# Performance work log

Measured on AMD Instinct MI355X. Metric: run time of the kernel, lower is better.

## Reference

```python
import jax, jax.numpy as jnp
import numpy as np

VOL_SHAPE = (256, 256, 256)
DELTA = 1
EPS = 1e-8


def _radius_bins(shape, delta):
    # Frequency-index radius map (equivalent to distance from DC with fft wraparound),
    # binned into shells of width `delta`. Computed once with numpy (constant).
    axes = [np.fft.fftfreq(n) * n for n in shape]
    grids = np.meshgrid(*axes, indexing='ij')
    r = np.sqrt(sum(g.astype(np.float64) ** 2 for g in grids))
    bins = np.floor(r / delta).astype(np.int32)
    return bins.ravel(), int(bins.max()) + 1

_BINS, _NUM_SHELLS = _radius_bins(VOL_SHAPE, DELTA)
_BINS_J = jnp.asarray(_BINS)


def setup_inputs() -> dict:
    key = jax.random.key(0)
    kx, ky = jax.random.split(key)
    shp = (2, 1) + VOL_SHAPE
    X = jax.random.normal(kx, shp, dtype=jnp.float32)
    Y = jax.random.normal(ky, shp, dtype=jnp.float32)
    return {"X": X, "Y": Y}


def _fsc(X, Y):
    B, C = X.shape[0], X.shape[1]
    Fx = jnp.fft.fftn(X, axes=(-3, -2, -1))  # complex64 [B,C,D,H,W]
    Fy = jnp.fft.fftn(Y, axes=(-3, -2, -1))
    N = VOL_SHAPE[0] * VOL_SHAPE[1] * VOL_SHAPE[2]
    # Per-voxel quantities, flattened over the volume: [B*C, N]
    num = (Fx.real * Fy.real + Fx.imag * Fy.imag).reshape(B * C, N)  # Re(Fx * conj(Fy))
    px = (Fx.real ** 2 + Fx.imag ** 2).reshape(B * C, N)
    py = (Fy.real ** 2 + Fy.imag ** 2).reshape(B * C, N)
    seg = lambda v: jax.ops.segment_sum(v, _BINS_J, num_segments=_NUM_SHELLS)
    num_s = jax.vmap(seg)(num)  # [B*C, S]
    px_s = jax.vmap(seg)(px)
    py_s = jax.vmap(seg)(py)
    fsc = num_s / jnp.sqrt(px_s * py_s + EPS)  # [B*C, S]
    return fsc.reshape(B, C, _NUM_SHELLS)


def reference(X, Y):
    fsc = _fsc(X, Y)
    # size_average=True: average over radii, channel and batch -> scalar
    return jnp.mean(fsc)
```

## Files before the change

### kernel.cpp

```cpp
#include <hip/hip_runtime.h>
#include <math.h>

#define VOL (256 * 256 * 256)
#define NSHELL 222
#define SBINS 224
#define NSPLIT 16
#define PI_D 3.14159265358979323846
#define VSTRIDE ((size_t)129 << 16)

__global__ void tw_init(float2* __restrict__ gtw) {
  int t = threadIdx.x;
  double a = -2.0 * PI_D * (double)t / 256.0;
  gtw[t] = make_float2((float)cos(a), (float)sin(a));
}

__device__ __forceinline__ void seg_flush(float* sh, int sb, float nv, float pv,
                                          float qv, int l) {
#pragma unroll
  for (int d = 1; d < 64; d <<= 1) {
    int sbo = __shfl_down(sb, d);
    float no = __shfl_down(nv, d);
    float po = __shfl_down(pv, d);
    float qo = __shfl_down(qv, d);
    if (l + d < 64 && sbo == sb) { nv += no; pv += po; qv += qo; }
  }
  int sbp = __shfl_up(sb, 1);
  if (l == 0 || sbp != sb) {
    atomicAdd(&sh[3 * sb + 0], nv);
    atomicAdd(&sh[3 * sb + 1], pv);
    atomicAdd(&sh[3 * sb + 2], qv);
  }
}

__device__ __forceinline__ float2 cmul(float2 a, float2 b) {
  return make_float2(a.x * b.x - a.y * b.y, a.x * b.y + a.y * b.x);
}

__device__ __forceinline__ void fft16(float2* v) {
  const float C1 = 0.92387953251128674f;
  const float S1 = 0.38268343236508978f;
  const float R2 = 0.70710678118654752f;
  float2 s[16];
#pragma unroll
  for (int p = 0; p < 4; ++p) {
    float2 a = v[p], b = v[p + 4], cc = v[p + 8], d = v[p + 12];
    float2 t0 = make_float2(a.x + cc.x, a.y + cc.y);
    float2 t2 = make_float2(a.x - cc.x, a.y - cc.y);
    float2 t1 = make_float2(b.x + d.x, b.y + d.y);
    float2 t3 = make_float2(b.x - d.x, b.y - d.y);
    s[p]      = make_float2(t0.x + t1.x, t0.y + t1.y);
    s[p + 4]  = make_float2(t2.x + t3.y, t2.y - t3.x);
    s[p + 8]  = make_float2(t0.x - t1.x, t0.y - t1.y);
    s[p + 12] = make_float2(t2.x - t3.y, t2.y + t3.x);
  }
  s[5]  = cmul(s[5],  make_float2(C1, -S1));
  s[6]  = cmul(s[6],  make_float2(R2, -R2));
  s[7]  = cmul(s[7],  make_float2(S1, -C1));
  s[9]  = cmul(s[9],  make_float2(R2, -R2));
  s[10] = cmul(s[10], make_float2(0.f, -1.f));
  s[11] = cmul(s[11], make_float2(-R2, -R2));
  s[13] = cmul(s[13], make_float2(S1, -C1));
  s[14] = cmul(s[14], make_float2(-R2, -R2));
  s[15] = cmul(s[15], make_float2(-C1, S1));
#pragma unroll
  for (int r = 0; r < 4; ++r) {
    float2 u0 = s[4 * r], u1 = s[4 * r + 1], u2 = s[4 * r + 2], u3 = s[4 * r + 3];
    float2 e0 = make_float2(u0.x + u2.x, u0.y + u2.y);
    float2 e1 = make_float2(u0.x - u2.x, u0.y - u2.y);
    float2 o0 = make_float2(u1.x + u3.x, u1.y + u3.y);
    float2 o1 = make_float2(u1.x - u3.x, u1.y - u3.y);
    v[r]      = make_float2(e0.x + o0.x, e0.y + o0.y);
    v[4 + r]  = make_float2(e1.x + o1.y, e1.y - o1.x);
    v[8 + r]  = make_float2(e0.x - o0.x, e0.y - o0.y);
    v[12 + r] = make_float2(e1.x - o1.y, e1.y + o1.x);
  }
}

__global__ __launch_bounds__(256, 4) void fft_z_pack(const float* __restrict__ X,
                                                     const float* __restrict__ Y,
                                                     float2* __restrict__ Gx,
                                                     float2* __restrict__ Gy,
                                                     const float2* __restrict__ gtw) {
  __shared__ float2 zs[256 * 17];
  int t = threadIdx.x;
  int li = t >> 4, c = t & 15;
  int y = blockIdx.x >> 4;
  int x0 = (blockIdx.x & 15) << 4;
  const float4* xp = (const float4*)(X + (((size_t)(x0 + li)) << 16) + ((size_t)y << 8));
  const float4* yp = (const float4*)(Y + (((size_t)(x0 + li)) << 16) + ((size_t)y << 8));
#pragma unroll
  for (int it = 0; it < 4; ++it) {
    float4 a = xp[c + 16 * it];
    float4 b = yp[c + 16 * it];
    int z0 = 4 * c + 64 * it;
    zs[(z0 + 0) * 17 + li] = make_float2(a.x, b.x);
    zs[(z0 + 1) * 17 + li] = make_float2(a.y, b.y);
    zs[(z0 + 2) * 17 + li] = make_float2(a.z, b.z);
    zs[(z0 + 3) * 17 + li] = make_float2(a.w, b.w);
  }
  float2 v[16];
#pragma unroll
  for (int m = 0; m < 16; ++m) v[m] = zs[(16 * m + c) * 17 + li];
  fft16(v);
#pragma unroll
  for (int k1 = 1; k1 < 16; ++k1) v[k1] = cmul(v[k1], gtw[c * k1]);
#pragma unroll
  for (int k1 = 0; k1 < 16; ++k1) zs[(16 * c + ((k1 + c) & 15)) * 17 + li] = v[k1];
  float2 u[16];
#pragma unroll
  for (int j2 = 0; j2 < 16; ++j2) u[j2] = zs[(16 * j2 + ((c + j2) & 15)) * 17 + li];
  fft16(u);
#pragma unroll
  for (int k2 = 0; k2 < 16; ++k2) zs[(16 * k2 + c) * 17 + li] = u[k2];
  __syncthreads();
  int xo = t & 15, ko = t >> 4;
  float2* gx = Gx + ((size_t)y << 8) + (size_t)(x0 + xo);
  float2* gy = Gy + ((size_t)y << 8) + (size_t)(x0 + xo);
#pragma unroll
  for (int g = 0; g < 9; ++g) {
    int kz = 16 * g + ko;
    if (kz <= 128) {
      float2 a = zs[kz * 17 + xo];
      float2 b = zs[((256 - kz) & 255) * 17 + xo];
      size_t off = (size_t)kz << 16;
      gx[off] = make_float2(0.5f * (a.x + b.x), 0.5f * (a.y - b.y));
      gy[off] = make_float2(0.5f * (a.y + b.y), 0.5f * (b.x - a.x));
    }
  }
}

__global__ __launch_bounds__(256, 4) void fft_y(float2* __restrict__ G,
                                                const float2* __restrict__ gtw) {
  __shared__ float2 scr[16 * 273];
  int t = threadIdx.x;
  int xi = t & 15, h = t >> 4;
  int x0 = blockIdx.x << 4;
  int kz = blockIdx.y;
  float2* Gp = G + (size_t)blockIdx.z * VSTRIDE + ((size_t)kz << 16) + (size_t)(x0 + xi);
  float2 v[16];
#pragma unroll
  for (int m = 0; m < 16; ++m) v[m] = Gp[(size_t)((m << 4) | h) << 8];
  fft16(v);
#pragma unroll
  for (int k1 = 1; k1 < 16; ++k1) v[k1] = cmul(v[k1], gtw[h * k1]);
  int wb = xi * 273 + h * 17;
#pragma unroll
  for (int k1 = 0; k1 < 16; ++k1) scr[wb + k1] = v[k1];
  __syncthreads();
  float2 u[16];
  int rb = xi * 273 + h;
#pragma unroll
  for (int j2 = 0; j2 < 16; ++j2) u[j2] = scr[rb + j2 * 17];
  fft16(u);
#pragma unroll
  for (int k2 = 0; k2 < 16; ++k2) Gp[(size_t)((k2 << 4) | h) << 8] = u[k2];
}

__global__ __launch_bounds__(256, 4) void fft_x_reduce(const float2* __restrict__ G,
                                                       double* __restrict__ sums,
                                                       const float2* __restrict__ gtw) {
  __shared__ float2 pool[4672];
  __shared__ float sh[3 * SBINS];
  int t = threadIdx.x;
  for (int i = t; i < 3 * SBINS; i += 256) sh[i] = 0.f;
  int vol = t >> 7, tt = t & 127;
  int g = tt >> 4, c = tt & 15;
  int kz = blockIdx.y;
  int r0 = blockIdx.x << 3;
  const float2* Gp = G + (size_t)vol * VSTRIDE + ((size_t)kz << 16) + ((size_t)(r0 + g) << 8);
  float2 v[16];
#pragma unroll
  for (int m = 0; m < 16; ++m) v[m] = Gp[(m << 4) | c];
  fft16(v);
#pragma unroll
  for (int k1 = 1; k1 < 16; ++k1) v[k1] = cmul(v[k1], gtw[c * k1]);
  {
    int sbase = ((vol << 3) | g) * 280;
#pragma unroll
    for (int k1 = 0; k1 < 16; ++k1) pool[sbase + c * 17 + k1] = v[k1];
    float2 u[16];
#pragma unroll
    for (int j2 = 0; j2 < 16; ++j2) u[j2] = pool[sbase + j2 * 17 + c];
    fft16(u);
    __syncthreads();
    float2* A = pool + vol * 2336;
#pragma unroll
    for (int k2 = 0; k2 < 16; ++k2) {
      int kx = (k2 << 4) | c;
      A[kx * 9 + k2 + g] = u[k2];
    }
  }
  __syncthreads();
  int fz = kz - ((kz & 128) ? 256 : 0);
  int fz2 = fz * fz;
  int w = t >> 6, l = t & 63;
  const float2* Ax = pool;
  const float2* Ay = pool + 2336;
#pragma unroll
  for (int rr = 0; rr < 2; ++rr) {
    int row = (w << 1) | rr;
    int ky = r0 + row;
    int fy = ky - ((ky & 128) ? 256 : 0);
    int c2 = fy * fy + fz2;
#pragma unroll
    for (int pass = 0; pass < 2; ++pass) {
      int kx = (pass << 6) | l;
      float2 xv = Ax[kx * 9 + (kx >> 4) + row];
      float2 yv = Ay[kx * 9 + (kx >> 4) + row];
      float nv = xv.x * yv.x + xv.y * yv.y;
      float pv = xv.x * xv.x + xv.y * xv.y;
      float qv = yv.x * yv.x + yv.y * yv.y;
      if (kx != 0) {
        int mk = 256 - kx;
        float2 mx = Ax[mk * 9 + (mk >> 4) + row];
        float2 my = Ay[mk * 9 + (mk >> 4) + row];
        nv += mx.x * my.x + mx.y * my.y;
        pv += mx.x * mx.x + mx.y * mx.y;
        qv += my.x * my.x + my.y * my.y;
      }
      int m = kx * kx + c2;
      int sb = (int)sqrtf((float)m);
      while (sb * sb > m) --sb;
      while ((sb + 1) * (sb + 1) <= m) ++sb;
      seg_flush(sh, sb, nv, pv, qv, l);
    }
    if (l == 0) {
      float2 xv = Ax[128 * 9 + 8 + row];
      float2 yv = Ay[128 * 9 + 8 + row];
      int m = 16384 + c2;
      int sb = (int)sqrtf((float)m);
      while (sb * sb > m) --sb;
      while ((sb + 1) * (sb + 1) <= m) ++sb;
      atomicAdd(&sh[3 * sb + 0], xv.x * yv.x + xv.y * yv.y);
      atomicAdd(&sh[3 * sb + 1], xv.x * xv.x + xv.y * xv.y);
      atomicAdd(&sh[3 * sb + 2], yv.x * yv.x + yv.y * yv.y);
    }
  }
  __syncthreads();
  float wf = (kz == 0 || kz == 128) ? 1.f : 2.f;
  double* sp = sums + (size_t)(blockIdx.x & (NSPLIT - 1)) * (3 * SBINS);
  for (int i = t; i < 3 * SBINS; i += 256) {
    float vv = sh[i];
    if (vv != 0.f) atomicAdd(&sp[i], (double)(wf * vv));
  }
}

__global__ void finalize(const double* __restrict__ sums, float* __restrict__ out) {
  __shared__ double red[2 * 3 * SBINS];
  int t = threadIdx.x;
  for (int i = t; i < 2 * 3 * SBINS; i += 256) {
    int b = i / (3 * SBINS), k = i - b * (3 * SBINS);
    const double* s = sums + (size_t)b * NSPLIT * 3 * SBINS + k;
    double a = 0.0;
#pragma unroll
    for (int sp = 0; sp < NSPLIT; ++sp) a += s[(size_t)sp * 3 * SBINS];
    red[i] = a;
  }
  __syncthreads();
  if (t == 0) {
    double acc = 0.0;
    for (int b = 0; b < 2; ++b) {
      const double* s = red + b * 3 * SBINS;
      for (int k = 0; k < NSHELL; ++k)
        acc += s[3 * k] / sqrt(s[3 * k + 1] * s[3 * k + 2] + 1e-8);
    }
    out[0] = (float)(acc / (2.0 * (double)NSHELL));
  }
}

extern "C" void kernel_launch(void* const* d_in, const int* in_sizes, int n_in,
                              void* d_out, int out_size, void* d_ws, size_t ws_size,
                              hipStream_t stream) {
  const float* X = (const float*)d_in[0];
  const float* Y = (const float*)d_in[1];
  float2* Gx = (float2*)d_ws;
  float2* Gy = Gx + VSTRIDE;
  double* sums = (double*)((char*)d_ws + (size_t)2 * VSTRIDE * sizeof(float2));
  float2* gtw = (float2*)(sums + (size_t)2 * NSPLIT * 3 * SBINS);

  hipMemsetAsync(sums, 0, (size_t)2 * NSPLIT * 3 * SBINS * sizeof(double), stream);
  tw_init<<<1, 256, 0, stream>>>(gtw);

  for (int b = 0; b < 2; ++b) {
    fft_z_pack<<<4096, 256, 0, stream>>>(X + (size_t)b * VOL, Y + (size_t)b * VOL, Gx, Gy, gtw);
    fft_y<<<dim3(16, 129, 2), 256, 0, stream>>>(Gx, gtw);
    fft_x_reduce<<<dim3(32, 129), 256, 0, stream>>>(Gx, sums + (size_t)b * NSPLIT * 3 * SBINS, gtw);
  }
  finalize<<<1, 256, 0, stream>>>(sums, (float*)d_out);
}
```

Before: 603.6 us.

## Make FFT kernels persistent with register prefetch of the next tile

All three FFT stages become persistent grid-stride kernels over 1024 blocks. Each block prefetches the next tile's global data into registers while it computes the current tile, so load latency overlaps with compute. Twiddles are cached in LDS in the z and y passes, and __syncthreads is replaced by a manual lgkmcnt wait plus s_barrier. The z-pass load pattern also changes from float4 reads through an LDS transpose to strided scalar loads straight into registers. The prefetch buffer adds register pressure, and the new loads are less coalesced.

```diff
diff --git a/kernel.cpp b/kernel.cpp
--- a/kernel.cpp
+++ b/kernel.cpp
@@ -12,6 +12,11 @@
   int t = threadIdx.x;
   double a = -2.0 * PI_D * (double)t / 256.0;
   gtw[t] = make_float2((float)cos(a), (float)sin(a));
+}
+
+__device__ __forceinline__ void lds_barrier() {
+  asm volatile("s_waitcnt lgkmcnt(0)" ::: "memory");
+  __builtin_amdgcn_s_barrier();
 }
 
 __device__ __forceinline__ void seg_flush(float* sh, int sb, float nv, float pv,
@@ -82,78 +87,111 @@
                                                      float2* __restrict__ Gy,
                                                      const float2* __restrict__ gtw) {
   __shared__ float2 zs[256 * 17];
+  __shared__ float2 tws[256];
   int t = threadIdx.x;
   int li = t >> 4, c = t & 15;
-  int y = blockIdx.x >> 4;
-  int x0 = (blockIdx.x & 15) << 4;
-  const float4* xp = (const float4*)(X + (((size_t)(x0 + li)) << 16) + ((size_t)y << 8));
-  const float4* yp = (const float4*)(Y + (((size_t)(x0 + li)) << 16) + ((size_t)y << 8));
-#pragma unroll
-  for (int it = 0; it < 4; ++it) {
-    float4 a = xp[c + 16 * it];
-    float4 b = yp[c + 16 * it];
-    int z0 = 4 * c + 64 * it;
-    zs[(z0 + 0) * 17 + li] = make_float2(a.x, b.x);
-    zs[(z0 + 1) * 17 + li] = make_float2(a.y, b.y);
-    zs[(z0 + 2) * 17 + li] = make_float2(a.z, b.z);
-    zs[(z0 + 3) * 17 + li] = make_float2(a.w, b.w);
-  }
-  float2 v[16];
-#pragma unroll
-  for (int m = 0; m < 16; ++m) v[m] = zs[(16 * m + c) * 17 + li];
-  fft16(v);
-#pragma unroll
-  for (int k1 = 1; k1 < 16; ++k1) v[k1] = cmul(v[k1], gtw[c * k1]);
-#pragma unroll
-  for (int k1 = 0; k1 < 16; ++k1) zs[(16 * c + ((k1 + c) & 15)) * 17 + li] = v[k1];
-  float2 u[16];
-#pragma unroll
-  for (int j2 = 0; j2 < 16; ++j2) u[j2] = zs[(16 * j2 + ((c + j2) & 15)) * 17 + li];
-  fft16(u);
-#pragma unroll
-  for (int k2 = 0; k2 < 16; ++k2) zs[(16 * k2 + c) * 17 + li] = u[k2];
-  __syncthreads();
-  int xo = t & 15, ko = t >> 4;
-  float2* gx = Gx + ((size_t)y << 8) + (size_t)(x0 + xo);
-  float2* gy = Gy + ((size_t)y << 8) + (size_t)(x0 + xo);
-#pragma unroll
-  for (int g = 0; g < 9; ++g) {
-    int kz = 16 * g + ko;
-    if (kz <= 128) {
-      float2 a = zs[kz * 17 + xo];
-      float2 b = zs[((256 - kz) & 255) * 17 + xo];
-      size_t off = (size_t)kz << 16;
-      gx[off] = make_float2(0.5f * (a.x + b.x), 0.5f * (a.y - b.y));
-      gy[off] = make_float2(0.5f * (a.y + b.y), 0.5f * (b.x - a.x));
-    }
-  }
+  tws[t] = gtw[t];
+  const int NT = 4096, Gs = 1024;
+  int bid = blockIdx.x;
+  float2 pf[16];
+
+#define P1_LOAD(tile)                                                         \
+  do {                                                                        \
+    int yy = (tile) >> 4, xx = ((((tile) & 15) << 4) + li);                   \
+    const float* xb = X + ((size_t)xx << 16) + (yy << 8) + c;                 \
+    const float* yb = Y + ((size_t)xx << 16) + (yy << 8) + c;                 \
+    _Pragma("unroll") for (int m = 0; m < 16; ++m)                            \
+        pf[m] = make_float2(xb[m << 4], yb[m << 4]);                          \
+  } while (0)
+
+  P1_LOAD(bid);
+  lds_barrier();
+  for (int tile = bid; tile < NT; tile += Gs) {
+    float2 v[16];
+#pragma unroll
+    for (int m = 0; m < 16; ++m) v[m] = pf[m];
+    if (tile + Gs < NT) P1_LOAD(tile + Gs);
+    fft16(v);
+#pragma unroll
+    for (int k1 = 1; k1 < 16; ++k1) v[k1] = cmul(v[k1], tws[c * k1]);
+#pragma unroll
+    for (int k1 = 0; k1 < 16; ++k1) zs[(16 * c + ((k1 + c) & 15)) * 17 + li] = v[k1];
+    float2 u[16];
+#pragma unroll
+    for (int j2 = 0; j2 < 16; ++j2) u[j2] = zs[(16 * j2 + ((c + j2) & 15)) * 17 + li];
+    fft16(u);
+#pragma unroll
+    for (int k2 = 0; k2 < 16; ++k2) zs[(16 * k2 + c) * 17 + li] = u[k2];
+    lds_barrier();
+    {
+      int yy = tile >> 4, x0 = ((tile) & 15) << 4;
+      float2* gx = Gx + (yy << 8) + (x0 + c);
+      float2* gy = Gy + (yy << 8) + (x0 + c);
+#pragma unroll
+      for (int g = 0; g < 9; ++g) {
+        int kz = 16 * g + li;
+        if (kz <= 128) {
+          float2 a = zs[kz * 17 + c];
+          float2 b = zs[((256 - kz) & 255) * 17 + c];
+          size_t off = (size_t)kz << 16;
+          gx[off] = make_float2(0.5f * (a.x + b.x), 0.5f * (a.y - b.y));
+          gy[off] = make_float2(0.5f * (a.y + b.y), 0.5f * (b.x - a.x));
+        }
+      }
+    }
+    lds_barrier();
+  }
+#undef P1_LOAD
 }
 
 __global__ __launch_bounds__(256, 4) void fft_y(float2* __restrict__ G,
                                                 const float2* __restrict__ gtw) {
   __shared__ float2 scr[16 * 273];
+  __shared__ float2 tws[256];
   int t = threadIdx.x;
   int xi = t & 15, h = t >> 4;
-  int x0 = blockIdx.x << 4;
-  int kz = blockIdx.y;
-  float2* Gp = G + (size_t)blockIdx.z * VSTRIDE + ((size_t)kz << 16) + (size_t)(x0 + xi);
-  float2 v[16];
-#pragma unroll
-  for (int m = 0; m < 16; ++m) v[m] = Gp[(size_t)((m << 4) | h) << 8];
-  fft16(v);
-#pragma unroll
-  for (int k1 = 1; k1 < 16; ++k1) v[k1] = cmul(v[k1], gtw[h * k1]);
-  int wb = xi * 273 + h * 17;
-#pragma unroll
-  for (int k1 = 0; k1 < 16; ++k1) scr[wb + k1] = v[k1];
-  __syncthreads();
-  float2 u[16];
-  int rb = xi * 273 + h;
-#pragma unroll
-  for (int j2 = 0; j2 < 16; ++j2) u[j2] = scr[rb + j2 * 17];
-  fft16(u);
-#pragma unroll
-  for (int k2 = 0; k2 < 16; ++k2) Gp[(size_t)((k2 << 4) | h) << 8] = u[k2];
+  tws[t] = gtw[t];
+  const int NT = 2 * 129 * 16, Gs = 1024;
+  int bid = blockIdx.x;
+  float2 pf[16];
+
+#define P2_PTR(tile)                                                          \
+  (G + (size_t)((tile) >= 2064) * VSTRIDE +                                   \
+   ((size_t)((((tile) >= 2064) ? (tile) - 2064 : (tile)) >> 4) << 16) +       \
+   (size_t)((((tile) & 15) << 4) + xi))
+#define P2_LOAD(tile)                                                         \
+  do {                                                                        \
+    float2* Gp_ = P2_PTR(tile);                                               \
+    _Pragma("unroll") for (int m = 0; m < 16; ++m)                            \
+        pf[m] = Gp_[(size_t)((m << 4) | h) << 8];                             \
+  } while (0)
+
+  P2_LOAD(bid);
+  lds_barrier();
+  for (int tile = bid; tile < NT; tile += Gs) {
+    float2 v[16];
+#pragma unroll
+    for (int m = 0; m < 16; ++m) v[m] = pf[m];
+    if (tile + Gs < NT) P2_LOAD(tile + Gs);
+    fft16(v);
+#pragma unroll
+    for (int k1 = 1; k1 < 16; ++k1) v[k1] = cmul(v[k1], tws[h * k1]);
+    lds_barrier();
+    int wb = xi * 273 + h * 17;
+#pragma unroll
+    for (int k1 = 0; k1 < 16; ++k1) scr[wb + k1] = v[k1];
+    lds_barrier();
+    float2 u[16];
+    int rb = xi * 273 + h;
+#pragma unroll
+    for (int j2 = 0; j2 < 16; ++j2) u[j2] = scr[rb + j2 * 17];
+    fft16(u);
+    float2* Gp = P2_PTR(tile);
+#pragma unroll
+    for (int k2 = 0; k2 < 16; ++k2) Gp[(size_t)((k2 << 4) | h) << 8] = u[k2];
+  }
+#undef P2_LOAD
+#undef P2_PTR
 }
 
 __global__ __launch_bounds__(256, 4) void fft_x_reduce(const float2* __restrict__ G,
@@ -165,84 +203,105 @@
   for (int i = t; i < 3 * SBINS; i += 256) sh[i] = 0.f;
   int vol = t >> 7, tt = t & 127;
   int g = tt >> 4, c = tt & 15;
-  int kz = blockIdx.y;
-  int r0 = blockIdx.x << 3;
-  const float2* Gp = G + (size_t)vol * VSTRIDE + ((size_t)kz << 16) + ((size_t)(r0 + g) << 8);
-  float2 v[16];
-#pragma unroll
-  for (int m = 0; m < 16; ++m) v[m] = Gp[(m << 4) | c];
-  fft16(v);
-#pragma unroll
-  for (int k1 = 1; k1 < 16; ++k1) v[k1] = cmul(v[k1], gtw[c * k1]);
-  {
-    int sbase = ((vol << 3) | g) * 280;
-#pragma unroll
-    for (int k1 = 0; k1 < 16; ++k1) pool[sbase + c * 17 + k1] = v[k1];
+  const int NT = 129 * 32, Gs = 1024;
+  int bid = blockIdx.x;
+  float2 pf[16];
+
+#define P3_PTR(tile)                                                          \
+  (G + (size_t)vol * VSTRIDE + ((size_t)((tile) >> 5) << 16) +                \
+   ((size_t)((((tile) & 31) << 3) + g) << 8))
+#define P3_LOAD(tile)                                                         \
+  do {                                                                        \
+    const float2* Gp_ = P3_PTR(tile);                                         \
+    _Pragma("unroll") for (int m = 0; m < 16; ++m) pf[m] = Gp_[(m << 4) | c]; \
+  } while (0)
+
+  P3_LOAD(bid);
+  for (int tile = bid; tile < NT; tile += Gs) {
+    float2 v[16];
+#pragma unroll
+    for (int m = 0; m < 16; ++m) v[m] = pf[m];
+    if (tile + Gs < NT) P3_LOAD(tile + Gs);
+    fft16(v);
+#pragma unroll
+    for (int k1 = 1; k1 < 16; ++k1) v[k1] = cmul(v[k1], gtw[c * k1]);
+    lds_barrier();
     float2 u[16];
-#pragma unroll
-    for (int j2 = 0; j2 < 16; ++j2) u[j2] = pool[sbase + j2 * 17 + c];
-    fft16(u);
-    __syncthreads();
-    float2* A = pool + vol * 2336;
-#pragma unroll
-    for (int k2 = 0; k2 < 16; ++k2) {
-      int kx = (k2 << 4) | c;
-      A[kx * 9 + k2 + g] = u[k2];
-    }
-  }
-  __syncthreads();
-  int fz = kz - ((kz & 128) ? 256 : 0);
-  int fz2 = fz * fz;
-  int w = t >> 6, l = t & 63;
-  const float2* Ax = pool;
-  const float2* Ay = pool + 2336;
-#pragma unroll
-  for (int rr = 0; rr < 2; ++rr) {
-    int row = (w << 1) | rr;
-    int ky = r0 + row;
-    int fy = ky - ((ky & 128) ? 256 : 0);
-    int c2 = fy * fy + fz2;
-#pragma unroll
-    for (int pass = 0; pass < 2; ++pass) {
-      int kx = (pass << 6) | l;
-      float2 xv = Ax[kx * 9 + (kx >> 4) + row];
-      float2 yv = Ay[kx * 9 + (kx >> 4) + row];
-      float nv = xv.x * yv.x + xv.y * yv.y;
-      float pv = xv.x * xv.x + xv.y * xv.y;
-      float qv = yv.x * yv.x + yv.y * yv.y;
-      if (kx != 0) {
-        int mk = 256 - kx;
-        float2 mx = Ax[mk * 9 + (mk >> 4) + row];
-        float2 my = Ay[mk * 9 + (mk >> 4) + row];
-        nv += mx.x * my.x + mx.y * my.y;
-        pv += mx.x * mx.x + mx.y * mx.y;
-        qv += my.x * my.x + my.y * my.y;
+    {
+      int sbase = ((vol << 3) | g) * 280;
+#pragma unroll
+      for (int k1 = 0; k1 < 16; ++k1) pool[sbase + c * 17 + k1] = v[k1];
+#pragma unroll
+      for (int j2 = 0; j2 < 16; ++j2) u[j2] = pool[sbase + j2 * 17 + c];
+      fft16(u);
+    }
+    lds_barrier();
+    {
+      float2* A = pool + vol * 2336;
+#pragma unroll
+      for (int k2 = 0; k2 < 16; ++k2) {
+        int kx = (k2 << 4) | c;
+        A[kx * 9 + k2 + g] = u[k2];
       }
-      int m = kx * kx + c2;
-      int sb = (int)sqrtf((float)m);
-      while (sb * sb > m) --sb;
-      while ((sb + 1) * (sb + 1) <= m) ++sb;
-      seg_flush(sh, sb, nv, pv, qv, l);
-    }
-    if (l == 0) {
-      float2 xv = Ax[128 * 9 + 8 + row];
-      float2 yv = Ay[128 * 9 + 8 + row];
-      int m = 16384 + c2;
-      int sb = (int)sqrtf((float)m);
-      while (sb * sb > m) --sb;
-      while ((sb + 1) * (sb + 1) <= m) ++sb;
-      atomicAdd(&sh[3 * sb + 0], xv.x * yv.x + xv.y * yv.y);
-      atomicAdd(&sh[3 * sb + 1], xv.x * xv.x + xv.y * xv.y);
-      atomicAdd(&sh[3 * sb + 2], yv.x * yv.x + yv.y * yv.y);
-    }
-  }
-  __syncthreads();
-  float wf = (kz == 0 || kz == 128) ? 1.f : 2.f;
-  double* sp = sums + (size_t)(blockIdx.x & (NSPLIT - 1)) * (3 * SBINS);
-  for (int i = t; i < 3 * SBINS; i += 256) {
-    float vv = sh[i];
-    if (vv != 0.f) atomicAdd(&sp[i], (double)(wf * vv));
-  }
+    }
+    lds_barrier();
+    int kz = tile >> 5, rt = tile & 31;
+    int fz = kz - ((kz & 128) ? 256 : 0);
+    int fz2 = fz * fz;
+    int w = t >> 6, l = t & 63;
+    const float2* Ax = pool;
+    const float2* Ay = pool + 2336;
+#pragma unroll
+    for (int rr = 0; rr < 2; ++rr) {
+      int row = (w << 1) | rr;
+      int ky = (rt << 3) + row;
+      int fy = ky - ((ky & 128) ? 256 : 0);
+      int c2 = fy * fy + fz2;
+#pragma unroll
+      for (int pass = 0; pass < 2; ++pass) {
+        int kx = (pass << 6) | l;
+        float2 xv = Ax[kx * 9 + (kx >> 4) + row];
+        float2 yv = Ay[kx * 9 + (kx >> 4) + row];
+        float nv = xv.x * yv.x + xv.y * yv.y;
+        float pv = xv.x * xv.x + xv.y * xv.y;
+        float qv = yv.x * yv.x + yv.y * yv.y;
+        if (kx != 0) {
+          int mk = 256 - kx;
+          float2 mx = Ax[mk * 9 + (mk >> 4) + row];
+          float2 my = Ay[mk * 9 + (mk >> 4) + row];
+          nv += mx.x * my.x + mx.y * my.y;
+          pv += mx.x * mx.x + mx.y * mx.y;
+          qv += my.x * my.x + my.y * my.y;
+        }
+        int m = kx * kx + c2;
+        int sb = (int)sqrtf((float)m);
+        while (sb * sb > m) --sb;
+        while ((sb + 1) * (sb + 1) <= m) ++sb;
+        seg_flush(sh, sb, nv, pv, qv, l);
+      }
+      if (l == 0) {
+        float2 xv = Ax[128 * 9 + 8 + row];
+        float2 yv = Ay[128 * 9 + 8 + row];
+        int m = 16384 + c2;
+        int sb = (int)sqrtf((float)m);
+        while (sb * sb > m) --sb;
+        while ((sb + 1) * (sb + 1) <= m) ++sb;
+        atomicAdd(&sh[3 * sb + 0], xv.x * yv.x + xv.y * yv.y);
+        atomicAdd(&sh[3 * sb + 1], xv.x * xv.x + xv.y * xv.y);
+        atomicAdd(&sh[3 * sb + 2], yv.x * yv.x + yv.y * yv.y);
+      }
+    }
+    lds_barrier();
+    float wf = (kz == 0 || kz == 128) ? 1.f : 2.f;
+    double* sp = sums + (size_t)(tile & (NSPLIT - 1)) * (3 * SBINS);
+    for (int i = t; i < 3 * SBINS; i += 256) {
+      float vv = sh[i];
+      if (vv != 0.f) atomicAdd(&sp[i], (double)(wf * vv));
+      sh[i] = 0.f;
+    }
+  }
+#undef P3_LOAD
+#undef P3_PTR
 }
 
 __global__ void finalize(const double* __restrict__ sums, float* __restrict__ out) {
@@ -282,9 +341,9 @@
   tw_init<<<1, 256, 0, stream>>>(gtw);
 
   for (int b = 0; b < 2; ++b) {
-    fft_z_pack<<<4096, 256, 0, stream>>>(X + (size_t)b * VOL, Y + (size_t)b * VOL, Gx, Gy, gtw);
-    fft_y<<<dim3(16, 129, 2), 256, 0, stream>>>(Gx, gtw);
-    fft_x_reduce<<<dim3(32, 129), 256, 0, stream>>>(Gx, sums + (size_t)b * NSPLIT * 3 * SBINS, gtw);
+    fft_z_pack<<<1024, 256, 0, stream>>>(X + (size_t)b * VOL, Y + (size_t)b * VOL, Gx, Gy, gtw);
+    fft_y<<<1024, 256, 0, stream>>>(Gx, gtw);
+    fft_x_reduce<<<1024, 256, 0, stream>>>(Gx, sums + (size_t)b * NSPLIT * 3 * SBINS, gtw);
   }
   finalize<<<1, 256, 0, stream>>>(sums, (float*)d_out);
 }
```

Result: slower. 760.3 us (+26.0%).
